# Optimization experiments

Hardware: AMD Instinct MI355X
Metric: run time of the kernel (lower is better)

The kernel has to match this reference:

```python
import jax, jax.numpy as jnp
import numpy as np

BATCH = 8192
IN_FEATURES = 1024
OUT_FEATURES = 1024
GRID_SIZE = 5
SPLINE_ORDER = 3
GRID_MIN, GRID_MAX = -1.0, 1.0
NUM_BASES = GRID_SIZE + SPLINE_ORDER  # 8
GRID_LEN = GRID_SIZE + 2 * SPLINE_ORDER + 1  # 12


def setup_inputs() -> dict:
    key = jax.random.key(0)
    k1, k2, k3 = jax.random.split(key, 3)
    x = jax.random.normal(k1, (BATCH, IN_FEATURES), dtype=jnp.float32)
    base_weight = jax.random.normal(k2, (OUT_FEATURES, IN_FEATURES), dtype=jnp.float32) * 0.1
    spline_weight = jax.random.normal(k3, (OUT_FEATURES, IN_FEATURES, NUM_BASES), dtype=jnp.float32) * 0.1
    grid = jnp.linspace(GRID_MIN, GRID_MAX, GRID_LEN, dtype=jnp.float32)  # buffer, not learned
    return {"x": x, "base_weight": base_weight, "spline_weight": spline_weight, "grid": grid}


def _bspline_basis(xc, grid, order):
    """Iterative Cox-de Boor DP, vectorized over all features and basis indices.
    xc: [B, F] clamped inputs; grid: [G] uniform knots (all denominators > 0).
    Returns [B, F, G - order - 1] = [B, F, NUM_BASES]."""
    G = grid.shape[0]
    xe = xc[..., None]  # [B, F, 1]
    # k = 0: indicator of knot interval, matches (x >= grid[i]) & (x < grid[i+1])
    B = ((xe >= grid[:-1]) & (xe < grid[1:])).astype(xc.dtype)  # [B, F, G-1]
    for k in range(1, order + 1):
        left = (xe - grid[: G - k - 1]) / (grid[k : G - 1] - grid[: G - k - 1]) * B[..., :-1]
        right = (grid[k + 1 : G] - xe) / (grid[k + 1 : G] - grid[1 : G - k]) * B[..., 1:]
        B = left + right  # [B, F, G-1-k]
    return B


def reference(x, base_weight, spline_weight, grid):
    # base path: SiLU activation then linear
    base_output = jax.nn.silu(x) @ base_weight.T  # [B, out]
    # spline path: B-spline basis per feature, weighted sum over (in, basis)
    x_clamped = jnp.clip(x, GRID_MIN * 0.99, GRID_MAX * 0.99)
    basis = _bspline_basis(x_clamped, grid, SPLINE_ORDER)  # [B, in, NUM_BASES]
    spline_output = jnp.einsum("bin,oin->bo", basis, spline_weight)
    return base_output + spline_output
```

## Files before the change

### kernel.cpp

```cpp
#include <hip/hip_runtime.h>
#include <stdint.h>

typedef _Float16 f16;
typedef __attribute__((ext_vector_type(8))) _Float16 f16x8;
typedef __attribute__((ext_vector_type(4))) float f32x4;

#define BATCH 8192
#define INF   1024
#define OUTF  1024
#define KTOT  9216
#define NT    72
#define CONV_BLOCKS 4608

__device__ __forceinline__ void gload16(const void* g, void* l) {
  __builtin_amdgcn_global_load_lds(
      (const __attribute__((address_space(1))) uint32_t*)g,
      (__attribute__((address_space(3))) uint32_t*)l, 16, 0, 0);
}

__global__ __launch_bounds__(256) void fused_prep_kernel(
    const float* __restrict__ bw, const float* __restrict__ sw,
    const float* __restrict__ x, const float* __restrict__ grid,
    f16* __restrict__ Wb, f16* __restrict__ Abuf)
{
  int blk = blockIdx.x;
  if (blk < CONV_BLOCKS) {
    int idx = blk * 256 + threadIdx.x;
    int o = idx / 1152;
    int r = idx - o * 1152;
    int k8 = r * 8;
    const float* src = (k8 < INF) ? (bw + (size_t)o * INF + k8)
                                  : (sw + (size_t)o * (INF * 8) + (k8 - INF));
    float4 v0 = *(const float4*)src;
    float4 v1 = *(const float4*)(src + 4);
    f16x8 ov;
    ov[0] = (f16)v0.x; ov[1] = (f16)v0.y; ov[2] = (f16)v0.z; ov[3] = (f16)v0.w;
    ov[4] = (f16)v1.x; ov[5] = (f16)v1.y; ov[6] = (f16)v1.z; ov[7] = (f16)v1.w;
    *(f16x8*)(Wb + (size_t)o * KTOT + k8) = ov;
    return;
  }

  int q = (blk - CONV_BLOCKS) * 256 + threadIdx.x;
  int b = q >> 8;
  int i0 = (q & 255) << 2;
  float4 xv = *(const float4*)(x + ((size_t)b << 10) + i0);
  float xa[4] = {xv.x, xv.y, xv.z, xv.w};

  float g[12];
#pragma unroll
  for (int j = 0; j < 12; ++j) g[j] = grid[j];
  float H  = g[1] - g[0];
  float r1 = 1.0f / H;
  float r2 = 0.5f * r1;
  float r3 = (1.0f / 3.0f) * r1;

  f16 sil[4];
  f16x8 bas[4];
#pragma unroll
  for (int e = 0; e < 4; ++e) {
    float v = xa[e];
    sil[e] = (f16)(v / (1.0f + __expf(-v)));
    float xe = fminf(fmaxf(v, -0.99f), 0.99f);
    float Bv[11];
#pragma unroll
    for (int j = 0; j < 11; ++j) Bv[j] = (xe >= g[j] && xe < g[j + 1]) ? 1.0f : 0.0f;
#pragma unroll
    for (int j = 0; j < 10; ++j) Bv[j] = (xe - g[j]) * r1 * Bv[j] + (g[j + 2] - xe) * r1 * Bv[j + 1];
#pragma unroll
    for (int j = 0; j < 9; ++j)  Bv[j] = (xe - g[j]) * r2 * Bv[j] + (g[j + 3] - xe) * r2 * Bv[j + 1];
#pragma unroll
    for (int j = 0; j < 8; ++j)  Bv[j] = (xe - g[j]) * r3 * Bv[j] + (g[j + 4] - xe) * r3 * Bv[j + 1];
#pragma unroll
    for (int n = 0; n < 8; ++n) bas[e][n] = (f16)Bv[n];
  }
  f16* row = Abuf + (size_t)b * KTOT;
  *(uint64_t*)(row + i0) = *(const uint64_t*)sil;
  f16* bp = row + INF + (size_t)i0 * 8;
#pragma unroll
  for (int e = 0; e < 4; ++e) *(f16x8*)(bp + e * 8) = bas[e];
}

#define LDA(base, m, s) (*(const f16x8*)((base) + ((wr*128 + (m)*16 + la) * 64 + ((((s)*4 + lb) ^ lasw) * 8))))
#define LDB(base, n, s) (*(const f16x8*)((base) + ((wcn*64 + (n)*16 + la) * 64 + ((((s)*4 + lb) ^ lasw) * 8))))

#define MFMA1(m, n, s) acc[m][n] = __builtin_amdgcn_mfma_f32_16x16x32_f16(af[m][s], bf[n][s], acc[m][n], 0, 0, 0)
#define MFMA_S0(m0) do { \
  MFMA1(m0,0,0);   MFMA1(m0,1,0);   MFMA1(m0,2,0);   MFMA1(m0,3,0); \
  MFMA1(m0+1,0,0); MFMA1(m0+1,1,0); MFMA1(m0+1,2,0); MFMA1(m0+1,3,0); } while (0)
#define MFMA_S1(m0) do { \
  MFMA1(m0,0,1);   MFMA1(m0,1,1);   MFMA1(m0,2,1);   MFMA1(m0,3,1); \
  MFMA1(m0+1,0,1); MFMA1(m0+1,1,1); MFMA1(m0+1,2,1); MFMA1(m0+1,3,1); } while (0)

#define SCHED0 __builtin_amdgcn_sched_barrier(0)
#define SBARF do { __builtin_amdgcn_s_barrier(); SCHED0; } while (0)

template <bool ATOMIC>
__global__ __launch_bounds__(512, 2) void kan_gemm_kernel(
    const f16* __restrict__ A, const f16* __restrict__ W,
    float* __restrict__ C, float* __restrict__ P1)
{
  __shared__ __align__(16) f16 lsA[2 * 256 * 64];
  __shared__ __align__(16) f16 lsB[2 * 256 * 64];

  const size_t K = KTOT;
  int bid = blockIdx.x;
  int wg  = (bid & 7) * 32 + (bid >> 3);
  int tm  = wg & 31;
  int gg  = wg >> 5;
  int tn  = gg >> 1;
  int split = gg & 1;
  size_t kbase = (size_t)split * (NT * 64);

  int tid = threadIdx.x;
  int w = tid >> 6, l = tid & 63;
  int wr = w >> 2, wcn = w & 3;
  int la = l & 15, lb = l >> 4, lasw = la & 7;

  int rh = tid >> 3;
  int sc = (tid & 7) ^ (rh & 7);
  const f16* aSrc0 = A + (size_t)(tm * 256 + rh) * K + kbase + sc * 8;
  const f16* bSrc0 = W + (size_t)(tn * 256 + rh) * K + kbase + sc * 8;

  auto stage = [&](int h) {
    if (h >= 4 * NT) return;
    int tile = h >> 2, ty = h & 3, half = ty & 1;
    size_t koff = (size_t)tile * 64;
    if (ty < 2) {
      const f16* s = aSrc0 + (size_t)half * 128 * K + koff;
      f16* d = lsA + (tile & 1) * 16384 + half * 8192 + w * 512;
      gload16(s, d);
      gload16(s + 64 * K, d + 4096);
    } else {
      const f16* s = bSrc0 + (size_t)half * 128 * K + koff;
      f16* d = lsB + (tile & 1) * 16384 + half * 8192 + w * 512;
      gload16(s, d);
      gload16(s + 64 * K, d + 4096);
    }
  };

  f16x8 af[8][2], bf[4][2];
  f32x4 acc[8][4] = {};

  stage(2); stage(3); stage(0); stage(1); stage(6); stage(7);
  asm volatile("s_waitcnt vmcnt(4)" ::: "memory");
  SBARF;
  {
    const f16* bA = lsA; const f16* bB = lsB;
#pragma unroll
    for (int n = 0; n < 4; ++n) { bf[n][0] = LDB(bB, n, 0); bf[n][1] = LDB(bB, n, 1); }
    af[0][0] = LDA(bA, 0, 0); af[0][1] = LDA(bA, 0, 1);
    af[1][0] = LDA(bA, 1, 0); af[1][1] = LDA(bA, 1, 1);
  }

  for (int t = 0; t < NT; ++t) {
    const f16* bA  = lsA + (t & 1) * 16384;
    const f16* bB  = lsB + (t & 1) * 16384;
    const f16* bA1 = lsA + ((t + 1) & 1) * 16384;
    const f16* bB1 = lsB + ((t + 1) & 1) * 16384;
    int h1 = 4 * (t + 1), h2 = 4 * (t + 2);

    stage(h1 + 0); stage(h1 + 1);
    SBARF;
    __builtin_amdgcn_s_setprio(1);
    af[2][0] = LDA(bA, 2, 0); af[3][0] = LDA(bA, 3, 0);
    MFMA_S0(0);
    MFMA_S1(0);
    __builtin_amdgcn_s_setprio(0);
    af[2][1] = LDA(bA, 2, 1); af[3][1] = LDA(bA, 3, 1);
    SBARF;

    stage(h2 + 2);
    SBARF;
    __builtin_amdgcn_s_setprio(1);
    af[4][0] = LDA(bA, 4, 0); af[5][0] = LDA(bA, 5, 0);
    MFMA_S0(2);
    MFMA_S1(2);
    __builtin_amdgcn_s_setprio(0);
    af[4][1] = LDA(bA, 4, 1); af[5][1] = LDA(bA, 5, 1);
    SBARF;

    stage(h2 + 3);
    SBARF;
    __builtin_amdgcn_s_setprio(1);
    af[6][0] = LDA(bA, 6, 0); af[7][0] = LDA(bA, 7, 0);
    MFMA_S0(4);
    MFMA_S1(4);
    __builtin_amdgcn_s_setprio(0);
    af[6][1] = LDA(bA, 6, 1); af[7][1] = LDA(bA, 7, 1);
    SBARF;

    if (t < NT - 2)       asm volatile("s_waitcnt vmcnt(4)" ::: "memory");
    else if (t == NT - 2) asm volatile("s_waitcnt vmcnt(0)" ::: "memory");
    SBARF;
    __builtin_amdgcn_s_setprio(1);
    if (t < NT - 1) { af[0][0] = LDA(bA1, 0, 0); af[1][0] = LDA(bA1, 1, 0); }
    MFMA_S0(6);
    MFMA_S1(6);
    __builtin_amdgcn_s_setprio(0);
    if (t < NT - 1) {
#pragma unroll
      for (int n = 0; n < 4; ++n) bf[n][0] = LDB(bB1, n, 0);
#pragma unroll
      for (int n = 0; n < 4; ++n) bf[n][1] = LDB(bB1, n, 1);
      af[0][1] = LDA(bA1, 0, 1); af[1][1] = LDA(bA1, 1, 1);
    }
    SBARF;
  }

  int rowBase = tm * 256 + wr * 128 + lb * 4;
  int colBase = tn * 256 + wcn * 64 + la;
  float* dst = ATOMIC ? C : (split ? P1 : C);
#pragma unroll
  for (int m = 0; m < 8; ++m)
#pragma unroll
    for (int n = 0; n < 4; ++n) {
      int col = colBase + n * 16;
#pragma unroll
      for (int j = 0; j < 4; ++j) {
        int row = rowBase + m * 16 + j;
        if (ATOMIC) atomicAdd(&C[(size_t)row * OUTF + col], acc[m][n][j]);
        else        dst[(size_t)row * OUTF + col] = acc[m][n][j];
      }
    }
}

__global__ __launch_bounds__(256) void reduce_kernel(
    float* __restrict__ out, const float* __restrict__ p)
{
  size_t i = ((size_t)blockIdx.x * 256 + threadIdx.x) * 4;
  f32x4 a = *(f32x4*)(out + i);
  f32x4 b = *(const f32x4*)(p + i);
  a += b;
  *(f32x4*)(out + i) = a;
}

extern "C" void kernel_launch(void* const* d_in, const int* in_sizes, int n_in,
                              void* d_out, int out_size, void* d_ws, size_t ws_size,
                              hipStream_t stream)
{
  const float* x  = (const float*)d_in[0];
  const float* bw = (const float*)d_in[1];
  const float* sw = (const float*)d_in[2];
  const float* gr = (const float*)d_in[3];
  float* out = (float*)d_out;

  f16* Wb = (f16*)d_ws;
  size_t wBytes = (size_t)OUTF * KTOT * sizeof(f16);
  f16* Abuf = (f16*)((char*)d_ws + wBytes);
  size_t aBytes = (size_t)BATCH * KTOT * sizeof(f16);
  size_t oBytes = (size_t)BATCH * OUTF * sizeof(float);

  int prepBlocks = (BATCH * INF / 4) / 256;
  fused_prep_kernel<<<CONV_BLOCKS + prepBlocks, 256, 0, stream>>>(
      bw, sw, x, gr, Wb, Abuf);

  if (ws_size >= wBytes + aBytes + oBytes) {
    float* P1 = (float*)((char*)d_ws + wBytes + aBytes);
    kan_gemm_kernel<false><<<256, 512, 0, stream>>>(Abuf, Wb, out, P1);
    reduce_kernel<<<(int)(oBytes / sizeof(float) / 4 / 256), 256, 0, stream>>>(out, P1);
  } else {
    hipMemsetAsync(d_out, 0, oBytes, stream);
    kan_gemm_kernel<true><<<256, 512, 0, stream>>>(Abuf, Wb, out, nullptr);
  }
}
```

Measured before the change: 216.6 us.

## Switch GEMM inner loop to 32x32x16 MFMA tiles and remap workgroup-to-XCD assignment

Replaces the 16x16x32 f16 MFMA micro-tiles with 32x32x16 MFMAs, regrouping LDS fragment loads (A per k-substep, all B fragments loaded once per tile) and rewriting the epilogue for the 32x32 accumulator layout. This cuts the number of MFMA issues and LDS reads per K-tile. The block-to-tile mapping also changes so each XCD owns a contiguous group of M tiles across N tiles and splits, aiming at better L2 locality. The 32x32 layout changes the register and LDS access pattern, and the new mapping must still cover every (tm, tn, split) exactly once.

```diff
diff --git a/kernel.cpp b/kernel.cpp
--- a/kernel.cpp
+++ b/kernel.cpp
@@ -4,6 +4,7 @@
 typedef _Float16 f16;
 typedef __attribute__((ext_vector_type(8))) _Float16 f16x8;
 typedef __attribute__((ext_vector_type(4))) float f32x4;
+typedef __attribute__((ext_vector_type(16))) float f32x16;
 
 #define BATCH 8192
 #define INF   1024
@@ -80,19 +81,32 @@
   for (int e = 0; e < 4; ++e) *(f16x8*)(bp + e * 8) = bas[e];
 }
 
-#define LDA(base, m, s) (*(const f16x8*)((base) + ((wr*128 + (m)*16 + la) * 64 + ((((s)*4 + lb) ^ lasw) * 8))))
-#define LDB(base, n, s) (*(const f16x8*)((base) + ((wcn*64 + (n)*16 + la) * 64 + ((((s)*4 + lb) ^ lasw) * 8))))
-
-#define MFMA1(m, n, s) acc[m][n] = __builtin_amdgcn_mfma_f32_16x16x32_f16(af[m][s], bf[n][s], acc[m][n], 0, 0, 0)
-#define MFMA_S0(m0) do { \
-  MFMA1(m0,0,0);   MFMA1(m0,1,0);   MFMA1(m0,2,0);   MFMA1(m0,3,0); \
-  MFMA1(m0+1,0,0); MFMA1(m0+1,1,0); MFMA1(m0+1,2,0); MFMA1(m0+1,3,0); } while (0)
-#define MFMA_S1(m0) do { \
-  MFMA1(m0,0,1);   MFMA1(m0,1,1);   MFMA1(m0,2,1);   MFMA1(m0,3,1); \
-  MFMA1(m0+1,0,1); MFMA1(m0+1,1,1); MFMA1(m0+1,2,1); MFMA1(m0+1,3,1); } while (0)
+#define LDA32(base, m, ks) (*(const f16x8*)((base) + (wr*128 + (m)*32 + l31)*64 + ((((ks)*2 + l5) ^ l7) * 8)))
+#define LDB32(base, n, ks) (*(const f16x8*)((base) + (wcn*64 + (n)*32 + l31)*64 + ((((ks)*2 + l5) ^ l7) * 8)))
+
+#define MFMA8(s, kk) do { \
+  acc[0][0] = __builtin_amdgcn_mfma_f32_32x32x16_f16(af[s][0], bfk[kk][0], acc[0][0], 0, 0, 0); \
+  acc[1][0] = __builtin_amdgcn_mfma_f32_32x32x16_f16(af[s][1], bfk[kk][0], acc[1][0], 0, 0, 0); \
+  acc[2][0] = __builtin_amdgcn_mfma_f32_32x32x16_f16(af[s][2], bfk[kk][0], acc[2][0], 0, 0, 0); \
+  acc[3][0] = __builtin_amdgcn_mfma_f32_32x32x16_f16(af[s][3], bfk[kk][0], acc[3][0], 0, 0, 0); \
+  acc[0][1] = __builtin_amdgcn_mfma_f32_32x32x16_f16(af[s][0], bfk[kk][1], acc[0][1], 0, 0, 0); \
+  acc[1][1] = __builtin_amdgcn_mfma_f32_32x32x16_f16(af[s][1], bfk[kk][1], acc[1][1], 0, 0, 0); \
+  acc[2][1] = __builtin_amdgcn_mfma_f32_32x32x16_f16(af[s][2], bfk[kk][1], acc[2][1], 0, 0, 0); \
+  acc[3][1] = __builtin_amdgcn_mfma_f32_32x32x16_f16(af[s][3], bfk[kk][1], acc[3][1], 0, 0, 0); \
+} while (0)
+
+#define READS_A(s, ks, bA_) do { \
+  af[s][0] = LDA32(bA_, 0, ks); af[s][1] = LDA32(bA_, 1, ks); \
+  af[s][2] = LDA32(bA_, 2, ks); af[s][3] = LDA32(bA_, 3, ks); } while (0)
+
+#define READS_B_ALL(bB_) do { \
+  bfk[0][0] = LDB32(bB_, 0, 0); bfk[0][1] = LDB32(bB_, 1, 0); \
+  bfk[1][0] = LDB32(bB_, 0, 1); bfk[1][1] = LDB32(bB_, 1, 1); \
+  bfk[2][0] = LDB32(bB_, 0, 2); bfk[2][1] = LDB32(bB_, 1, 2); \
+  bfk[3][0] = LDB32(bB_, 0, 3); bfk[3][1] = LDB32(bB_, 1, 3); } while (0)
 
 #define SCHED0 __builtin_amdgcn_sched_barrier(0)
-#define SBARF do { __builtin_amdgcn_s_barrier(); SCHED0; } while (0)
+#define SBARF  do { __builtin_amdgcn_s_barrier(); SCHED0; } while (0)
 
 template <bool ATOMIC>
 __global__ __launch_bounds__(512, 2) void kan_gemm_kernel(
@@ -104,17 +118,17 @@
 
   const size_t K = KTOT;
   int bid = blockIdx.x;
-  int wg  = (bid & 7) * 32 + (bid >> 3);
-  int tm  = wg & 31;
-  int gg  = wg >> 5;
-  int tn  = gg >> 1;
-  int split = gg & 1;
+  int xcd = bid & 7;
+  int u   = bid >> 3;
+  int tm  = xcd * 4 + (u & 3);
+  int tn  = (u >> 2) & 3;
+  int split = u >> 4;
   size_t kbase = (size_t)split * (NT * 64);
 
   int tid = threadIdx.x;
   int w = tid >> 6, l = tid & 63;
   int wr = w >> 2, wcn = w & 3;
-  int la = l & 15, lb = l >> 4, lasw = la & 7;
+  int l31 = l & 31, l5 = l >> 5, l7 = l & 7;
 
   int rh = tid >> 3;
   int sc = (tid & 7) ^ (rh & 7);
@@ -138,23 +152,19 @@
     }
   };
 
-  f16x8 af[8][2], bf[4][2];
-  f32x4 acc[8][4] = {};
+  f16x8 af[2][4];
+  f16x8 bfk[4][2];
+  f32x16 acc[4][2] = {};
 
   stage(2); stage(3); stage(0); stage(1); stage(6); stage(7);
   asm volatile("s_waitcnt vmcnt(4)" ::: "memory");
   SBARF;
-  {
-    const f16* bA = lsA; const f16* bB = lsB;
-#pragma unroll
-    for (int n = 0; n < 4; ++n) { bf[n][0] = LDB(bB, n, 0); bf[n][1] = LDB(bB, n, 1); }
-    af[0][0] = LDA(bA, 0, 0); af[0][1] = LDA(bA, 0, 1);
-    af[1][0] = LDA(bA, 1, 0); af[1][1] = LDA(bA, 1, 1);
-  }
+  READS_B_ALL(lsB);
+  READS_A(0, 0, lsA);
+  READS_A(1, 1, lsA);
 
   for (int t = 0; t < NT; ++t) {
     const f16* bA  = lsA + (t & 1) * 16384;
-    const f16* bB  = lsB + (t & 1) * 16384;
     const f16* bA1 = lsA + ((t + 1) & 1) * 16384;
     const f16* bB1 = lsB + ((t + 1) & 1) * 16384;
     int h1 = 4 * (t + 1), h2 = 4 * (t + 2);
@@ -162,64 +172,53 @@
     stage(h1 + 0); stage(h1 + 1);
     SBARF;
     __builtin_amdgcn_s_setprio(1);
-    af[2][0] = LDA(bA, 2, 0); af[3][0] = LDA(bA, 3, 0);
-    MFMA_S0(0);
-    MFMA_S1(0);
-    __builtin_amdgcn_s_setprio(0);
-    af[2][1] = LDA(bA, 2, 1); af[3][1] = LDA(bA, 3, 1);
+    MFMA8(0, 0);
+    __builtin_amdgcn_s_setprio(0);
+    READS_A(0, 2, bA);
     SBARF;
 
     stage(h2 + 2);
     SBARF;
     __builtin_amdgcn_s_setprio(1);
-    af[4][0] = LDA(bA, 4, 0); af[5][0] = LDA(bA, 5, 0);
-    MFMA_S0(2);
-    MFMA_S1(2);
-    __builtin_amdgcn_s_setprio(0);
-    af[4][1] = LDA(bA, 4, 1); af[5][1] = LDA(bA, 5, 1);
+    MFMA8(1, 1);
+    __builtin_amdgcn_s_setprio(0);
+    READS_A(1, 3, bA);
     SBARF;
 
     stage(h2 + 3);
     SBARF;
     __builtin_amdgcn_s_setprio(1);
-    af[6][0] = LDA(bA, 6, 0); af[7][0] = LDA(bA, 7, 0);
-    MFMA_S0(4);
-    MFMA_S1(4);
-    __builtin_amdgcn_s_setprio(0);
-    af[6][1] = LDA(bA, 6, 1); af[7][1] = LDA(bA, 7, 1);
+    MFMA8(0, 2);
+    __builtin_amdgcn_s_setprio(0);
     SBARF;
 
     if (t < NT - 2)       asm volatile("s_waitcnt vmcnt(4)" ::: "memory");
     else if (t == NT - 2) asm volatile("s_waitcnt vmcnt(0)" ::: "memory");
     SBARF;
     __builtin_amdgcn_s_setprio(1);
-    if (t < NT - 1) { af[0][0] = LDA(bA1, 0, 0); af[1][0] = LDA(bA1, 1, 0); }
-    MFMA_S0(6);
-    MFMA_S1(6);
+    MFMA8(1, 3);
     __builtin_amdgcn_s_setprio(0);
     if (t < NT - 1) {
-#pragma unroll
-      for (int n = 0; n < 4; ++n) bf[n][0] = LDB(bB1, n, 0);
-#pragma unroll
-      for (int n = 0; n < 4; ++n) bf[n][1] = LDB(bB1, n, 1);
-      af[0][1] = LDA(bA1, 0, 1); af[1][1] = LDA(bA1, 1, 1);
+      READS_B_ALL(bB1);
+      READS_A(0, 0, bA1);
+      READS_A(1, 1, bA1);
     }
     SBARF;
   }
 
-  int rowBase = tm * 256 + wr * 128 + lb * 4;
-  int colBase = tn * 256 + wcn * 64 + la;
+  int colBase  = tn * 256 + wcn * 64 + l31;
+  int rowBase0 = tm * 256 + wr * 128 + 4 * l5;
   float* dst = ATOMIC ? C : (split ? P1 : C);
 #pragma unroll
-  for (int m = 0; m < 8; ++m)
-#pragma unroll
-    for (int n = 0; n < 4; ++n) {
-      int col = colBase + n * 16;
-#pragma unroll
-      for (int j = 0; j < 4; ++j) {
-        int row = rowBase + m * 16 + j;
-        if (ATOMIC) atomicAdd(&C[(size_t)row * OUTF + col], acc[m][n][j]);
-        else        dst[(size_t)row * OUTF + col] = acc[m][n][j];
+  for (int m = 0; m < 4; ++m)
+#pragma unroll
+    for (int n = 0; n < 2; ++n) {
+      int col = colBase + n * 32;
+#pragma unroll
+      for (int r = 0; r < 16; ++r) {
+        int row = rowBase0 + m * 32 + (r & 3) + 8 * (r >> 2);
+        if (ATOMIC) atomicAdd(&dst[(size_t)row * OUTF + col], acc[m][n][r]);
+        else        dst[(size_t)row * OUTF + col] = acc[m][n][r];
       }
     }
 }
```

New measurement: 226.8 us. 1.05x slower.
